# Optimization experiments

Measured on AMD Instinct MI355X. Metric: run time of the kernel, lower is better.

## Reference

```python
import jax, jax.numpy as jnp
import numpy as np

K = 11  # masked conv3d kernel size

def mask_A(k):
    # mask type 'A': flattened (i,j,t) positions with current_id < k^3//2 + 1
    # (current_id starts at 1) -> first k^3//2 positions are 1.
    m = (np.arange(k ** 3) < (k ** 3) // 2).astype(np.float32).reshape(k, k, k)
    return jnp.asarray(m)

def conv3d(x, w, b, pad):
    out = jax.lax.conv_general_dilated(
        x, w, window_strides=(1, 1, 1), padding=[(pad, pad)] * 3,
        dimension_numbers=('NCDHW', 'OIDHW', 'NCDHW'))
    return out + b[None, :, None, None, None]

def conv2d(x, w, b, pad):
    out = jax.lax.conv_general_dilated(
        x, w, window_strides=(1, 1), padding=[(pad, pad)] * 2,
        dimension_numbers=('NCHW', 'OIHW', 'NCHW'))
    return out + b[None, :, None, None]

def pconv(x, w, b):
    # 1x1x1 conv3d as channel GEMM; w: [O, C]
    return jnp.einsum('bcdhw,oc->bodhw', x, w) + b[None, :, None, None, None]

def _phi(z):
    return 0.5 * (1.0 + jax.lax.erf(z / jnp.sqrt(2.0).astype(z.dtype)))

def setup_inputs() -> dict:
    key = jax.random.key(0)
    ks = jax.random.split(key, 12)
    M = 192
    B, H, W = 1, 48, 48
    s = 0.02
    x = jax.random.normal(ks[0], (B, M, H, W), jnp.float32)
    hyper = jax.random.normal(ks[1], (B, 2 * M, H, W), jnp.float32)
    W3 = s * jax.random.normal(ks[2], (M, 2 * M, 3, 3), jnp.float32)
    b3 = jnp.zeros((M,), jnp.float32)
    W1 = s * jax.random.normal(ks[3], (24, 1, K, K, K), jnp.float32)
    b1 = jnp.zeros((24,), jnp.float32)
    Wa = s * jax.random.normal(ks[4], (48, 25), jnp.float32)
    ba = jnp.zeros((48,), jnp.float32)
    Wb = s * jax.random.normal(ks[5], (96, 48), jnp.float32)
    bb = jnp.zeros((96,), jnp.float32)
    Wc = s * jax.random.normal(ks[6], (9, 96), jnp.float32)
    bc = jnp.zeros((9,), jnp.float32)
    return {"x": x, "hyper": hyper, "W3": W3, "b3": b3, "W1": W1, "b1": b1,
            "Wa": Wa, "ba": ba, "Wb": Wb, "bb": bb, "Wc": Wc, "bc": bc}

def reference(x, hyper, W3, b3, W1, b1, Wa, ba, Wb, bb, Wc, bc):
    # x: [B,M,H,W], hyper: [B,2M,H,W]
    x5 = x[:, None]                                   # [B,1,M,H,W]
    h = conv2d(hyper, W3, b3, 1)[:, None]             # [B,1,M,H,W]
    W1m = W1 * mask_A(K)[None, None]                  # causal mask re-applied each fwd
    x1 = conv3d(x5, W1m, b1, 5)                       # [B,24,M,H,W]
    t = jnp.concatenate([x1, h], axis=1)              # [B,25,M,H,W]
    t = jax.nn.relu(pconv(t, Wa, ba))                 # [B,48,M,H,W]
    t = jax.nn.relu(pconv(t, Wb, bb))                 # [B,96,M,H,W]
    out = pconv(t, Wc, bc)                            # [B,9,M,H,W]
    # 3-component weighted Gaussian entropy model
    mu = out[:, 0:3]
    sc = out[:, 3:6]
    sc = jnp.abs(jnp.where(sc == 0.0, 1e-9, sc))
    w = jax.nn.softmax(out[:, 6:9], axis=1)
    xe = x[:, None]                                   # [B,1,M,H,W]
    lik = jnp.abs(_phi((xe + 0.5 - mu) / sc) - _phi((xe - 0.5 - mu) / sc))
    p3 = jnp.sum(w * lik, axis=1)                     # [B,M,H,W]
    return (p3, out)
```

## Files before the change

kernel.cpp:

```cpp
#include <hip/hip_runtime.h>
#include <hip/hip_fp16.h>
#include <math.h>

#define HW    2304
#define NPOS  442368

typedef _Float16 f16x8 __attribute__((ext_vector_type(8)));
typedef float    f32x4 __attribute__((ext_vector_type(4)));

__device__ __forceinline__ float phi_f(float z) {
    return 0.5f * (1.0f + erff(z * 0.70710678118654752f));
}
__device__ __forceinline__ unsigned short f2h(float v) {
    _Float16 h = (_Float16)v;
    return *reinterpret_cast<unsigned short*>(&h);
}
__device__ __forceinline__ unsigned int pk2(float a, float b) {
    return (unsigned int)f2h(a) | ((unsigned int)f2h(b) << 16);
}

__global__ __launch_bounds__(256) void prep_hyperT(const float* __restrict__ hyper,
                                                   unsigned short* __restrict__ hyperTp) {
    __shared__ float s[32][33];
    const int pt = blockIdx.x, it = blockIdx.y;
    const int tid = threadIdx.x;
    const int c = tid & 31, r = tid >> 5;
    const int pp = pt * 32 + c;
    const int yp = pp / 50, xp = pp % 50;
    const bool inter = (pp < 2500) && yp >= 1 && yp <= 48 && xp >= 1 && xp <= 48;
    const int src = inter ? ((yp - 1) * 48 + (xp - 1)) : 0;
#pragma unroll
    for (int i = 0; i < 4; ++i) {
        int icl = r + i * 8;
        s[icl][c] = inter ? hyper[(size_t)(it * 32 + icl) * HW + src] : 0.f;
    }
    __syncthreads();
#pragma unroll
    for (int i = 0; i < 4; ++i) {
        int pl = r + i * 8;
        int pp2 = pt * 32 + pl;
        if (pp2 < 2500)
            hyperTp[(size_t)pp2 * 384 + it * 32 + c] = f2h(s[c][pl]);
    }
}

__global__ __launch_bounds__(256) void prep_misc(const float* __restrict__ W3,
                                                 const float* __restrict__ W1,
                                                 const float* __restrict__ Wa,
                                                 const float* __restrict__ ba,
                                                 const float* __restrict__ b1,
                                                 const float* __restrict__ Wb,
                                                 const float* __restrict__ bb,
                                                 const float* __restrict__ Wc,
                                                 const float* __restrict__ xg,
                                                 unsigned short* __restrict__ apack,
                                                 unsigned short* __restrict__ pk,
                                                 unsigned short* __restrict__ xh) {
    const int bx = blockIdx.x;
    if (bx < 2592) {
        int idx = bx * 256 + threadIdx.x;
        int j = idx & 7;
        int l = (idx >> 3) & 63;
        int rest = idx >> 9;
        int t = rest % 9; rest /= 9;
        int c = rest % 12; int T = rest / 12;
        int oc = T * 16 + (l & 15);
        int ic = c * 32 + (l >> 4) * 8 + j;
        apack[idx] = f2h(W3[((size_t)oc * 384 + ic) * 9 + t]);
    } else if (bx < 2752) {
        int idx = (bx - 2592) * 256 + threadIdx.x;
        if (idx >= 40960) return;
        float v = 0.f;
        if (idx < 31744) {
            int j = idx & 7, lane = (idx >> 3) & 63, s = (idx >> 9) & 1, c = idx >> 10;
            int q = lane >> 4;
            int oc = s * 16 + (lane & 15);
            int r = 2 * c + (q >> 1), h = q & 1, kw = 8 * h + j;
            if (oc < 24 && r < 61 && kw < 11) {
                int kd = r / 11, kh = r % 11;
                int tap = kd * 121 + kh * 11 + kw;
                if (tap < 665) v = W1[oc * 1331 + tap];
            }
        } else if (idx < 33280) {
            int i2 = idx - 31744;
            int j = i2 & 7, lane = (i2 >> 3) & 63, t = i2 >> 9;
            int m = t * 16 + (lane & 15), k = (lane >> 4) * 8 + j;
            if (k < 25) v = Wa[m * 25 + k];
            else if (k == 25) {
                float s = ba[m];
                for (int c = 0; c < 24; ++c) s += Wa[m * 25 + c] * b1[c];
                v = s;
            }
        } else if (idx < 39424) {
            int i3 = idx - 33280;
            int j = i3 & 7, lane = (i3 >> 3) & 63, k2 = (i3 >> 9) & 1, s = i3 >> 10;
            int m = s * 16 + (lane & 15), ch = k2 * 32 + (lane >> 4) * 8 + j;
            if (ch < 48) v = Wb[m * 48 + ch];
            else if (ch == 48) v = bb[m];
        } else {
            int i4 = idx - 39424;
            int j = i4 & 7, lane = (i4 >> 3) & 63, k3 = i4 >> 9;
            int m = lane & 15, ch = k3 * 32 + (lane >> 4) * 8 + j;
            if (m < 9) v = Wc[m * 96 + ch];
        }
        pk[idx] = f2h(v);
    } else {
        int idx = (bx - 2752) * 256 + threadIdx.x;
        float4 f = ((const float4*)xg)[idx];
        *(uint2*)&xh[idx * 4] = make_uint2(pk2(f.x, f.y), pk2(f.z, f.w));
    }
}

__global__ __launch_bounds__(256) void conv2d_mfma(const unsigned short* __restrict__ hyperTp,
                                                   const unsigned short* __restrict__ apack,
                                                   const float* __restrict__ b3,
                                                   float* __restrict__ hbuf) {
    const int T = blockIdx.x;
    const int tid = threadIdx.x, w = tid >> 6, lane = tid & 63;
    const int n = lane & 15, q = lane >> 4;
    const int g0 = blockIdx.y * 8 + w * 2;
    int yy[2], xb[2]; size_t base[2];
#pragma unroll
    for (int j = 0; j < 2; ++j) {
        int g = g0 + j;
        yy[j] = g / 3; xb[j] = (g % 3) * 16;
        base[j] = (size_t)(yy[j] * 50 + xb[j] + n) * 384 + q * 8;
    }
    f32x4 acc[2] = {};
    for (int c = 0; c < 12; ++c) {
        const unsigned short* ap = apack + ((size_t)(T * 12 + c) * 9) * 512 + lane * 8;
        const int coff = c * 32;
#pragma unroll
        for (int t = 0; t < 9; ++t) {
            f16x8 a = *(const f16x8*)(ap + t * 512);
            const int dd = (t / 3) * 50 + (t % 3);
#pragma unroll
            for (int j = 0; j < 2; ++j) {
                f16x8 b = *(const f16x8*)(hyperTp + base[j] + (size_t)dd * 384 + coff);
                acc[j] = __builtin_amdgcn_mfma_f32_16x16x32_f16(a, b, acc[j], 0, 0, 0);
            }
        }
    }
#pragma unroll
    for (int j = 0; j < 2; ++j)
#pragma unroll
        for (int e = 0; e < 4; ++e) {
            int oc = T * 16 + q * 4 + e;
            hbuf[(size_t)oc * HW + yy[j] * 48 + xb[j] + n] = acc[j][e] + b3[oc];
        }
}

__global__ __launch_bounds__(128) void conv3d_mfma(const unsigned short* __restrict__ xh,
                                                   const unsigned short* __restrict__ pk,
                                                   unsigned short* __restrict__ t0g) {
    __shared__ unsigned short P[4096];
    const int tid = threadIdx.x, w = tid >> 6, lane = tid & 63;
    const int n = lane & 15, q = lane >> 4;
    const int x0 = blockIdx.x * 4, y0 = blockIdx.y * 2, d0 = blockIdx.z * 16;

    for (int k = 0; k < 32; ++k) {
        int i = tid + k * 128;
        if (i < 4032) {
            int py = i / 336, r = i - py * 336, pz = r >> 4, xx = r & 15;
            int gz = d0 - 5 + pz, gy = y0 - 5 + py, gx = x0 - 5 + xx;
            unsigned short v = 0;
            if (gz >= 0 && gy >= 0 && gy < 48 && gx >= 0 && gx < 48)
                v = xh[(size_t)gz * HW + gy * 48 + gx];
            P[i] = v;
        }
    }
    __syncthreads();

    const f32x4 zf = {0.f, 0.f, 0.f, 0.f};
    f32x4 acc[4][2];
#pragma unroll
    for (int p = 0; p < 4; ++p) { acc[p][0] = zf; acc[p][1] = zf; }

    const f16x8* Av = (const f16x8*)pk;
    f16x8 a0 = Av[lane], a1 = Av[64 + lane];
    for (int c = 0; c < 31; ++c) {
        f16x8 ca0 = a0, ca1 = a1;
        int cn = (c < 30) ? c + 1 : 30;
        a0 = Av[cn * 128 + lane];
        a1 = Av[cn * 128 + 64 + lane];
        int r = 2 * c + (q >> 1);
        int kd = r / 11, kh = r - kd * 11;
        const unsigned short* rowp = P + ((w + kh) * 336 + (n + kd) * 16 + (q & 1) * 8);
        unsigned int u[6];
        *(uint4*)&u[0] = *(const uint4*)(rowp);
        *(uint2*)&u[4] = *(const uint2*)(rowp + 8);
#pragma unroll
        for (int px = 0; px < 4; ++px) {
            unsigned int bw[4];
#pragma unroll
            for (int i = 0; i < 4; ++i) {
                if ((px & 1) == 0) bw[i] = u[(px >> 1) + i];
                else bw[i] = (u[(px >> 1) + i] >> 16) | (u[(px >> 1) + 1 + i] << 16);
            }
            f16x8 bf = *(f16x8*)bw;
            acc[px][0] = __builtin_amdgcn_mfma_f32_16x16x32_f16(ca0, bf, acc[px][0], 0, 0, 0);
            acc[px][1] = __builtin_amdgcn_mfma_f32_16x16x32_f16(ca1, bf, acc[px][1], 0, 0, 0);
        }
    }
    __syncthreads();

#pragma unroll
    for (int px = 0; px < 4; ++px) {
        unsigned int lo = pk2(acc[px][0][0], acc[px][0][1]);
        unsigned int hi = pk2(acc[px][0][2], acc[px][0][3]);
        *(uint2*)&P[(w * 16 + n) * 96 + px * 24 + q * 4] = make_uint2(lo, hi);
        if (q < 2) {
            unsigned int l2 = pk2(acc[px][1][0], acc[px][1][1]);
            unsigned int h2 = pk2(acc[px][1][2], acc[px][1][3]);
            *(uint2*)&P[(w * 16 + n) * 96 + px * 24 + 16 + q * 4] = make_uint2(l2, h2);
        }
    }
    __syncthreads();
#pragma unroll
    for (int k = 0; k < 3; ++k) {
        int idx4 = tid + k * 128;
        int row = idx4 / 12, w12 = idx4 - row * 12;
        int px = w12 / 3, third = w12 - px * 3;
        int dep = row & 15, wv = row >> 4;
        uint4 v = *(const uint4*)&P[row * 96 + px * 24 + third * 8];
        size_t pos = (size_t)(d0 + dep) * HW + (y0 + wv) * 48 + x0 + px;
        ((uint4*)t0g)[pos * 3 + third] = v;
    }
}

__global__ __launch_bounds__(128) void mlp_lik(const unsigned short* __restrict__ t0g,
                                               const float* __restrict__ hbuf,
                                               const float* __restrict__ xg,
                                               const unsigned short* __restrict__ pk,
                                               const float* __restrict__ bc,
                                               float* __restrict__ out) {
    __shared__ unsigned short t1s[2][32 * 72];
    __shared__ unsigned short t2s[2][32 * 104];
    __shared__ float oacs[2][32 * 13];
    const int tid = threadIdx.x, wv = tid >> 6, lane = tid & 63;
    const int n = lane & 15, q = lane >> 4;

    const f16x8* WaF = (const f16x8*)(pk + 31744);
    const f16x8* WbF = (const f16x8*)(pk + 33280);
    const f16x8* WcF = (const f16x8*)(pk + 39424);
    f16x8 waf[3], wbf[12], wcf[3];
#pragma unroll
    for (int s = 0; s < 3; ++s) waf[s] = WaF[s * 64 + lane];
#pragma unroll
    for (int t = 0; t < 12; ++t) wbf[t] = WbF[t * 64 + lane];
#pragma unroll
    for (int k = 0; k < 3; ++k) wcf[k] = WcF[k * 64 + lane];
    float bcv[4];
#pragma unroll
    for (int e = 0; e < 4; ++e) bcv[e] = (q * 4 + e < 9) ? bc[q * 4 + e] : 0.f;

#pragma unroll
    for (int j = 0; j < 2; ++j) {
        unsigned int lo = (q == 0) ? 0x00003C00u : 0u;
        *(uint2*)&t1s[wv][(j * 16 + n) * 72 + 48 + q * 4] = make_uint2(lo, 0u);
    }

    const f32x4 zf = {0.f, 0.f, 0.f, 0.f};
    const f16x8 z8 = {};
    const int pw0 = blockIdx.x * 256 + wv * 128;

    for (int r = 0; r < 4; ++r) {
        const int p0 = pw0 + r * 32;
        f16x8 b0[2];
#pragma unroll
        for (int j = 0; j < 2; ++j) {
            b0[j] = (q < 3) ? *(const f16x8*)(t0g + (size_t)(p0 + j * 16 + n) * 24 + q * 8)
                            : z8;
            if (q == 3) {
                float hv = hbuf[p0 + j * 16 + n];
                b0[j][0] = (_Float16)hv; b0[j][1] = (_Float16)1.0f;
            }
        }
#pragma unroll
        for (int j = 0; j < 2; ++j)
#pragma unroll
            for (int s = 0; s < 3; ++s) {
                f32x4 r1 = __builtin_amdgcn_mfma_f32_16x16x32_f16(waf[s], b0[j], zf, 0, 0, 0);
                *(uint2*)&t1s[wv][(j * 16 + n) * 72 + s * 16 + q * 4] =
                    make_uint2(pk2(fmaxf(r1[0], 0.f), fmaxf(r1[1], 0.f)),
                               pk2(fmaxf(r1[2], 0.f), fmaxf(r1[3], 0.f)));
            }
#pragma unroll
        for (int j = 0; j < 2; ++j) {
            f32x4 rb[6];
#pragma unroll
            for (int s = 0; s < 6; ++s) rb[s] = zf;
#pragma unroll
            for (int k2 = 0; k2 < 2; ++k2) {
                f16x8 bf = *(const f16x8*)&t1s[wv][(j * 16 + n) * 72 + k2 * 32 + q * 8];
#pragma unroll
                for (int s = 0; s < 6; ++s)
                    rb[s] = __builtin_amdgcn_mfma_f32_16x16x32_f16(wbf[s * 2 + k2], bf, rb[s], 0, 0, 0);
            }
#pragma unroll
            for (int s = 0; s < 6; ++s)
                *(uint2*)&t2s[wv][(j * 16 + n) * 104 + s * 16 + q * 4] =
                    make_uint2(pk2(fmaxf(rb[s][0], 0.f), fmaxf(rb[s][1], 0.f)),
                               pk2(fmaxf(rb[s][2], 0.f), fmaxf(rb[s][3], 0.f)));
        }
#pragma unroll
        for (int j = 0; j < 2; ++j) {
            f32x4 rc = zf;
#pragma unroll
            for (int k3 = 0; k3 < 3; ++k3) {
                f16x8 bf = *(const f16x8*)&t2s[wv][(j * 16 + n) * 104 + k3 * 32 + q * 8];
                rc = __builtin_amdgcn_mfma_f32_16x16x32_f16(wcf[k3], bf, rc, 0, 0, 0);
            }
#pragma unroll
            for (int e = 0; e < 4; ++e) {
                int row = q * 4 + e;
                if (row < 9) oacs[wv][(j * 16 + n) * 13 + row] = rc[e] + bcv[e];
            }
        }
        if (lane < 32) {
            float o[9];
#pragma unroll
            for (int jj = 0; jj < 9; ++jj) o[jj] = oacs[wv][lane * 13 + jj];
            const int gp = p0 + lane;
            float xv = xg[gp];
            float m = fmaxf(o[6], fmaxf(o[7], o[8]));
            float e0 = expf(o[6] - m), e1 = expf(o[7] - m), e2 = expf(o[8] - m);
            float inv_es = 1.0f / (e0 + e1 + e2);
            float p = 0.f;
#pragma unroll
            for (int jj = 0; jj < 3; ++jj) {
                float mu = o[jj];
                float sc = o[3 + jj];
                sc = (sc == 0.0f) ? 1e-9f : sc;
                sc = fabsf(sc);
                float a = phi_f((xv + 0.5f - mu) / sc);
                float b = phi_f((xv - 0.5f - mu) / sc);
                float lik = fabsf(a - b);
                float wgt = ((jj == 0) ? e0 : (jj == 1) ? e1 : e2) * inv_es;
                p = fmaf(wgt, lik, p);
            }
            out[gp] = p;
#pragma unroll
            for (int jj = 0; jj < 9; ++jj) out[NPOS + (size_t)jj * NPOS + gp] = o[jj];
        }
    }
}

extern "C" void kernel_launch(void* const* d_in, const int* in_sizes, int n_in,
                              void* d_out, int out_size, void* d_ws, size_t ws_size,
                              hipStream_t stream) {
    const float* x     = (const float*)d_in[0];
    const float* hyper = (const float*)d_in[1];
    const float* W3    = (const float*)d_in[2];
    const float* b3    = (const float*)d_in[3];
    const float* W1    = (const float*)d_in[4];
    const float* b1    = (const float*)d_in[5];
    const float* Wa    = (const float*)d_in[6];
    const float* ba    = (const float*)d_in[7];
    const float* Wb    = (const float*)d_in[8];
    const float* bb    = (const float*)d_in[9];
    const float* Wc    = (const float*)d_in[10];
    const float* bc    = (const float*)d_in[11];
    float* out = (float*)d_out;

    float* hbuf = (float*)d_ws;
    unsigned short* hyperTp = (unsigned short*)(hbuf + NPOS);
    unsigned short* apack   = hyperTp + 960000;
    unsigned short* pk      = apack + 663552;
    unsigned short* xh      = pk + 40960;
    unsigned short* t0g     = xh + NPOS;

    prep_hyperT<<<dim3(79, 12), 256, 0, stream>>>(hyper, hyperTp);
    prep_misc<<<3184, 256, 0, stream>>>(W3, W1, Wa, ba, b1, Wb, bb, Wc, x,
                                        apack, pk, xh);
    conv2d_mfma<<<dim3(12, 18), 256, 0, stream>>>(hyperTp, apack, b3, hbuf);
    conv3d_mfma<<<dim3(12, 24, 12), 128, 0, stream>>>(xh, pk, t0g);
    mlp_lik<<<1728, 128, 0, stream>>>(t0g, hbuf, x, pk, bc, out);
}
```

Measured before the change: 184.1 us.

## Pre-pad fp16 input volume, vectorize conv3d halo loads, enlarge tiles

The x-to-fp16 prep now writes a zero-padded volume with a 64-wide row pitch. This lets conv3d load its shared-memory halo with aligned 16-byte vector loads instead of bounds-checked scalar gathers. conv3d blocks grow to 256 threads covering four y rows, so the halo is shared across more output rows. conv2d is split across twice as many blocks with one tile per wave, trading per-wave reuse for more parallelism. The MLP also switches its fp16 packing to the round-toward-zero pack intrinsic, which slightly changes rounding.

Measured after the change: 180.0 us. 2.2% less time.

```diff
diff --git a/kernel.cpp b/kernel.cpp
--- a/kernel.cpp
+++ b/kernel.cpp
@@ -6,6 +6,7 @@
 #define NPOS  442368
 
 typedef _Float16 f16x8 __attribute__((ext_vector_type(8)));
+typedef __fp16   h16x2 __attribute__((ext_vector_type(2)));
 typedef float    f32x4 __attribute__((ext_vector_type(4)));
 
 __device__ __forceinline__ float phi_f(float z) {
@@ -17,6 +18,10 @@
 }
 __device__ __forceinline__ unsigned int pk2(float a, float b) {
     return (unsigned int)f2h(a) | ((unsigned int)f2h(b) << 16);
+}
+__device__ __forceinline__ unsigned int pkrtz(float a, float b) {
+    h16x2 h = __builtin_amdgcn_cvt_pkrtz(a, b);
+    return *reinterpret_cast<unsigned int*>(&h);
 }
 
 __global__ __launch_bounds__(256) void prep_hyperT(const float* __restrict__ hyper,
@@ -55,7 +60,7 @@
                                                  const float* __restrict__ xg,
                                                  unsigned short* __restrict__ apack,
                                                  unsigned short* __restrict__ pk,
-                                                 unsigned short* __restrict__ xh) {
+                                                 unsigned short* __restrict__ xhp) {
     const int bx = blockIdx.x;
     if (bx < 2592) {
         int idx = bx * 256 + threadIdx.x;
@@ -106,8 +111,18 @@
         pk[idx] = f2h(v);
     } else {
         int idx = (bx - 2752) * 256 + threadIdx.x;
-        float4 f = ((const float4*)xg)[idx];
-        *(uint2*)&xh[idx * 4] = make_uint2(pk2(f.x, f.y), pk2(f.z, f.w));
+        if (idx >= 187456) return;
+        int si = idx * 4;
+        int zp = si / 3712, rem = si - zp * 3712;
+        int yp = rem >> 6, xp0 = rem & 63;
+        float f[4];
+#pragma unroll
+        for (int k = 0; k < 4; ++k) {
+            int xp = xp0 + k;
+            bool in = zp >= 5 && zp < 197 && yp >= 5 && yp < 53 && xp >= 5 && xp < 53;
+            f[k] = in ? xg[(size_t)(zp - 5) * HW + (yp - 5) * 48 + (xp - 5)] : 0.f;
+        }
+        *(uint2*)&xhp[si] = make_uint2(pk2(f[0], f[1]), pk2(f[2], f[3]));
     }
 }
 
@@ -118,15 +133,11 @@
     const int T = blockIdx.x;
     const int tid = threadIdx.x, w = tid >> 6, lane = tid & 63;
     const int n = lane & 15, q = lane >> 4;
-    const int g0 = blockIdx.y * 8 + w * 2;
-    int yy[2], xb[2]; size_t base[2];
-#pragma unroll
-    for (int j = 0; j < 2; ++j) {
-        int g = g0 + j;
-        yy[j] = g / 3; xb[j] = (g % 3) * 16;
-        base[j] = (size_t)(yy[j] * 50 + xb[j] + n) * 384 + q * 8;
-    }
-    f32x4 acc[2] = {};
+    const int g = blockIdx.y * 4 + w;
+    const int yy = g / 3, xb = (g % 3) * 16;
+    const size_t base = (size_t)(yy * 50 + xb + n) * 384 + q * 8;
+
+    f32x4 acc = {};
     for (int c = 0; c < 12; ++c) {
         const unsigned short* ap = apack + ((size_t)(T * 12 + c) * 9) * 512 + lane * 8;
         const int coff = c * 32;
@@ -134,39 +145,34 @@
         for (int t = 0; t < 9; ++t) {
             f16x8 a = *(const f16x8*)(ap + t * 512);
             const int dd = (t / 3) * 50 + (t % 3);
-#pragma unroll
-            for (int j = 0; j < 2; ++j) {
-                f16x8 b = *(const f16x8*)(hyperTp + base[j] + (size_t)dd * 384 + coff);
-                acc[j] = __builtin_amdgcn_mfma_f32_16x16x32_f16(a, b, acc[j], 0, 0, 0);
-            }
-        }
-    }
-#pragma unroll
-    for (int j = 0; j < 2; ++j)
-#pragma unroll
-        for (int e = 0; e < 4; ++e) {
-            int oc = T * 16 + q * 4 + e;
-            hbuf[(size_t)oc * HW + yy[j] * 48 + xb[j] + n] = acc[j][e] + b3[oc];
-        }
-}
-
-__global__ __launch_bounds__(128) void conv3d_mfma(const unsigned short* __restrict__ xh,
+            f16x8 b = *(const f16x8*)(hyperTp + base + (size_t)dd * 384 + coff);
+            acc = __builtin_amdgcn_mfma_f32_16x16x32_f16(a, b, acc, 0, 0, 0);
+        }
+    }
+#pragma unroll
+    for (int e = 0; e < 4; ++e) {
+        int oc = T * 16 + q * 4 + e;
+        hbuf[(size_t)oc * HW + yy * 48 + xb + n] = acc[e] + b3[oc];
+    }
+}
+
+__global__ __launch_bounds__(256) void conv3d_mfma(const unsigned short* __restrict__ xhp,
                                                    const unsigned short* __restrict__ pk,
                                                    unsigned short* __restrict__ t0g) {
-    __shared__ unsigned short P[4096];
+    __shared__ unsigned short P[6208];
     const int tid = threadIdx.x, w = tid >> 6, lane = tid & 63;
     const int n = lane & 15, q = lane >> 4;
-    const int x0 = blockIdx.x * 4, y0 = blockIdx.y * 2, d0 = blockIdx.z * 16;
-
-    for (int k = 0; k < 32; ++k) {
-        int i = tid + k * 128;
-        if (i < 4032) {
-            int py = i / 336, r = i - py * 336, pz = r >> 4, xx = r & 15;
-            int gz = d0 - 5 + pz, gy = y0 - 5 + py, gx = x0 - 5 + xx;
-            unsigned short v = 0;
-            if (gz >= 0 && gy >= 0 && gy < 48 && gx >= 0 && gx < 48)
-                v = xh[(size_t)gz * HW + gy * 48 + gx];
-            P[i] = v;
+    const int x0 = blockIdx.x * 4, y0 = blockIdx.y * 4, d0 = blockIdx.z * 16;
+
+#pragma unroll
+    for (int k = 0; k < 3; ++k) {
+        int idx = tid + k * 256;
+        if (idx < 588) {
+            int row = idx >> 1, half = idx & 1;
+            int py = row / 21, pz = row - py * 21;
+            const uint4* src = (const uint4*)(xhp + ((size_t)(d0 + pz) * 58 + (y0 + py)) * 64
+                                              + x0 + half * 8);
+            *(uint4*)&P[row * 16 + half * 8] = *src;
         }
     }
     __syncthreads();
@@ -185,7 +191,7 @@
         a1 = Av[cn * 128 + 64 + lane];
         int r = 2 * c + (q >> 1);
         int kd = r / 11, kh = r - kd * 11;
-        const unsigned short* rowp = P + ((w + kh) * 336 + (n + kd) * 16 + (q & 1) * 8);
+        const unsigned short* rowp = P + ((w + kh) * 21 + (n + kd)) * 16 + (q & 1) * 8;
         unsigned int u[6];
         *(uint4*)&u[0] = *(const uint4*)(rowp);
         *(uint2*)&u[4] = *(const uint2*)(rowp + 8);
@@ -218,7 +224,7 @@
     __syncthreads();
 #pragma unroll
     for (int k = 0; k < 3; ++k) {
-        int idx4 = tid + k * 128;
+        int idx4 = tid + k * 256;
         int row = idx4 / 12, w12 = idx4 - row * 12;
         int px = w12 / 3, third = w12 - px * 3;
         int dep = row & 15, wv = row >> 4;
@@ -282,8 +288,8 @@
             for (int s = 0; s < 3; ++s) {
                 f32x4 r1 = __builtin_amdgcn_mfma_f32_16x16x32_f16(waf[s], b0[j], zf, 0, 0, 0);
                 *(uint2*)&t1s[wv][(j * 16 + n) * 72 + s * 16 + q * 4] =
-                    make_uint2(pk2(fmaxf(r1[0], 0.f), fmaxf(r1[1], 0.f)),
-                               pk2(fmaxf(r1[2], 0.f), fmaxf(r1[3], 0.f)));
+                    make_uint2(pkrtz(fmaxf(r1[0], 0.f), fmaxf(r1[1], 0.f)),
+                               pkrtz(fmaxf(r1[2], 0.f), fmaxf(r1[3], 0.f)));
             }
 #pragma unroll
         for (int j = 0; j < 2; ++j) {
@@ -300,8 +306,8 @@
 #pragma unroll
             for (int s = 0; s < 6; ++s)
                 *(uint2*)&t2s[wv][(j * 16 + n) * 104 + s * 16 + q * 4] =
-                    make_uint2(pk2(fmaxf(rb[s][0], 0.f), fmaxf(rb[s][1], 0.f)),
-                               pk2(fmaxf(rb[s][2], 0.f), fmaxf(rb[s][3], 0.f)));
+                    make_uint2(pkrtz(fmaxf(rb[s][0], 0.f), fmaxf(rb[s][1], 0.f)),
+                               pkrtz(fmaxf(rb[s][2], 0.f), fmaxf(rb[s][3], 0.f)));
         }
 #pragma unroll
         for (int j = 0; j < 2; ++j) {
@@ -367,13 +373,13 @@
     unsigned short* hyperTp = (unsigned short*)(hbuf + NPOS);
     unsigned short* apack   = hyperTp + 960000;
     unsigned short* pk      = apack + 663552;
-    unsigned short* xh      = pk + 40960;
-    unsigned short* t0g     = xh + NPOS;
+    unsigned short* xhp     = pk + 40960;
+    unsigned short* t0g     = xhp + 749824;
 
     prep_hyperT<<<dim3(79, 12), 256, 0, stream>>>(hyper, hyperTp);
-    prep_misc<<<3184, 256, 0, stream>>>(W3, W1, Wa, ba, b1, Wb, bb, Wc, x,
-                                        apack, pk, xh);
-    conv2d_mfma<<<dim3(12, 18), 256, 0, stream>>>(hyperTp, apack, b3, hbuf);
-    conv3d_mfma<<<dim3(12, 24, 12), 128, 0, stream>>>(xh, pk, t0g);
+    prep_misc<<<3485, 256, 0, stream>>>(W3, W1, Wa, ba, b1, Wb, bb, Wc, x,
+                                        apack, pk, xhp);
+    conv2d_mfma<<<dim3(12, 36), 256, 0, stream>>>(hyperTp, apack, b3, hbuf);
+    conv3d_mfma<<<dim3(12, 12, 12), 256, 0, stream>>>(xhp, pk, t0g);
     mlp_lik<<<1728, 128, 0, stream>>>(t0g, hbuf, x, pk, bc, out);
 }
```
